# Performance work log

Measured on AMD Instinct MI355X. Metric: run time of the kernel, lower is better.

Reference implementation:

```python
import jax, jax.numpy as jnp
import numpy as np

CHUNK = 32
HEADS = 4
EPS_RMS = 1e-5

def silu(x):
    return jax.nn.silu(x)

def l2norm(x, eps=1e-6):
    return x * jax.lax.rsqrt(jnp.sum(x * x, axis=-1, keepdims=True) + eps)

def short_conv(x, w):
    # x: (b, l, c); w: (c, K) depthwise causal conv, no bias
    K = w.shape[1]
    L = x.shape[1]
    xp = jnp.pad(x, ((0, 0), (K - 1, 0), (0, 0)))
    out = xp[:, 0:L, :] * w[:, 0]
    for k in range(1, K):
        out = out + xp[:, k:k + L, :] * w[:, k]
    return out

def delta_rule_chunkwise(q, k, v, beta, chunk=CHUNK):
    # q,k: (b,h,l,dk); v: (b,h,l,dv); beta: (b,h,l). l divisible by chunk.
    b, h, l, dk = q.shape
    dv = v.shape[-1]
    n = l // chunk
    q = l2norm(q)
    k = l2norm(k)
    v = v * beta[..., None]
    k_beta = k * beta[..., None]
    resh = lambda x: x.reshape(b, h, n, chunk, -1)
    q, k, v, k_beta = map(resh, (q, k, v, k_beta))
    strict_lower = jnp.tril(jnp.ones((chunk, chunk), bool), -1)
    # A = -(k_beta k^T) kept strictly lower triangular
    attn = jnp.where(strict_lower, -(k_beta @ jnp.swapaxes(k, -1, -2)), 0.0)
    # forward substitution: T = (I - A)^{-1} - I built row by row (fixed 32 rows)
    for i in range(1, chunk):
        row = attn[..., i, :]                                  # (b,h,n,c)
        new = attn[..., i, :i] + jnp.einsum('...j,...jk->...k', row, attn[..., :, :i])
        attn = attn.at[..., i, :i].set(new)
    attn = attn + jnp.eye(chunk, dtype=attn.dtype)
    u = attn @ v        # (b,h,n,c,dv)
    w = attn @ k_beta   # (b,h,n,c,dk)
    lower_incl = jnp.tril(jnp.ones((chunk, chunk), bool))
    qc, kc, uc, wc = [jnp.moveaxis(x, 2, 0) for x in (q, k, u, w)]
    S0 = jnp.zeros((b, h, dk, dv), q.dtype)
    def step(S, inp):
        q_i, k_i, u_i, w_i = inp
        attn_i = jnp.where(lower_incl, q_i @ jnp.swapaxes(k_i, -1, -2), 0.0)
        u_adj = u_i - w_i @ S
        o_i = q_i @ S + attn_i @ u_adj
        S = S + jnp.swapaxes(k_i, -1, -2) @ u_adj
        return S, o_i
    S, o = jax.lax.scan(step, S0, (qc, kc, uc, wc))
    o = jnp.moveaxis(o, 0, 2).reshape(b, h, l, dv)
    return o, S

def ema_rule(v, gamma):
    # v: (b,h,l,dv), gamma: (b,h,l); sequential EMA scan
    v_t = jnp.moveaxis(v, 2, 0)       # (l,b,h,dv)
    g_t = jnp.moveaxis(gamma, 2, 0)   # (l,b,h)
    s0 = jnp.zeros(v.shape[:2] + (v.shape[-1],), v.dtype)
    def step(s, inp):
        vt, gt = inp
        s = gt[..., None] * s + (1.0 - gt[..., None]) * vt
        return s, s
    s_fin, out = jax.lax.scan(step, s0, (v_t, g_t))
    return jnp.moveaxis(out, 0, 2), s_fin

def rms_norm(x, w, eps=EPS_RMS):
    return x * jax.lax.rsqrt(jnp.mean(x * x, axis=-1, keepdims=True) + eps) * w

def setup_inputs() -> dict:
    key = jax.random.key(0)
    ks = jax.random.split(key, 16)
    b, l, d = 4, 2048, 1024
    H, conv_K = HEADS, 4
    s = 0.02
    return {
        'hidden_states': jax.random.normal(ks[0], (b, l, d), jnp.float32),
        'Wq': jax.random.normal(ks[1], (d, d), jnp.float32) * s,
        'Wk': jax.random.normal(ks[2], (d, d), jnp.float32) * s,
        'Wv': jax.random.normal(ks[3], (d, d), jnp.float32) * s,
        'conv_q': jax.random.normal(ks[4], (d, conv_K), jnp.float32) * 0.3,
        'conv_k': jax.random.normal(ks[5], (d, conv_K), jnp.float32) * 0.3,
        'conv_v': jax.random.normal(ks[6], (d, conv_K), jnp.float32) * 0.3,
        'Wb': jax.random.normal(ks[7], (d, H), jnp.float32) * s,
        'Wdec': jax.random.normal(ks[8], (d, H), jnp.float32) * s,
        'Wmix': jax.random.normal(ks[9], (d, H), jnp.float32) * s,
        'conv_mix': jax.random.normal(ks[10], (H, conv_K), jnp.float32) * 0.3,
        'mix_bias': jnp.full((H,), -2.0, jnp.float32),
        'rms_w': jnp.ones((d // H,), jnp.float32),
        'Wo': jax.random.normal(ks[11], (d, d), jnp.float32) * s,
    }

def reference(hidden_states, Wq, Wk, Wv, conv_q, conv_k, conv_v, Wb, Wdec, Wmix, conv_mix, mix_bias, rms_w, Wo):
    b, l, d = hidden_states.shape
    H = HEADS
    dk = d // H
    dv = d // H
    # projections + causal depthwise short conv (silu activation inside conv)
    q = silu(short_conv(hidden_states @ Wq, conv_q))
    k = silu(short_conv(hidden_states @ Wk, conv_k))
    v = silu(short_conv(hidden_states @ Wv, conv_v))
    mix_inp = silu(short_conv(hidden_states @ Wmix, conv_mix))  # (b,l,H)
    # qk_activation == 'silu' applies an extra silu after conv (per source)
    q = silu(q)
    k = silu(k)
    # split heads -> (b,H,l,dh)
    to_heads = lambda x, dh: jnp.transpose(x.reshape(b, l, H, dh), (0, 2, 1, 3))
    q_d = to_heads(q, dk)
    k_d = to_heads(k, dk)
    v_d = to_heads(v, dv)
    beta = jax.nn.sigmoid(hidden_states @ Wb)           # (b,l,H)
    beta_d = jnp.transpose(beta, (0, 2, 1))             # (b,H,l)
    o_d, S = delta_rule_chunkwise(q_d, k_d, v_d, beta_d)
    o_d = jnp.transpose(o_d, (0, 2, 1, 3))              # (b,l,H,dv)
    # EMA branch
    gamma = jax.nn.sigmoid(hidden_states @ Wdec)        # (b,l,H)
    gamma_d = jnp.transpose(gamma, (0, 2, 1))
    ema_out, ema_state = ema_rule(v_d, gamma_d)
    ema_out = jnp.transpose(ema_out, (0, 2, 1, 3))      # (b,l,H,dv)
    # fine-grained head mix gate
    mix = jax.nn.sigmoid(mix_inp + mix_bias)            # (b,l,H)
    o = (1.0 - mix[..., None]) * o_d + mix[..., None] * ema_out
    # per-head RMSNorm then output projection
    o = rms_norm(o, rms_w)
    out = o.reshape(b, l, H * dv) @ Wo
    return out
```

## Files before the change

### kernel.cpp

```cpp
#include <hip/hip_runtime.h>
#include <hip/hip_bf16.h>

#define B 4
#define L 2048
#define D 1024
#define NH 4
#define DK 256
#define CHUNK 32
#define NCH 64
#define BH (B*NH)
#define ET 64
#define ENCH (L/ET)
#define TB 8

typedef __attribute__((ext_vector_type(8))) __bf16 bf16x8;
typedef __attribute__((ext_vector_type(4))) __bf16 bf16x4;
typedef __attribute__((ext_vector_type(4))) float f32x4;

__device__ inline unsigned short f2bf(float f) {
    union { float f; unsigned u; } v; v.f = f;
    unsigned r = v.u + 0x7fffu + ((v.u >> 16) & 1u);
    return (unsigned short)(r >> 16);
}
__device__ inline float bf2f(unsigned short h) {
    union { unsigned u; float f; } v; v.u = ((unsigned)h) << 16; return v.f;
}
__device__ inline float sigmoidf_(float x) { return 1.0f / (1.0f + __expf(-x)); }
__device__ inline float siluf_(float x) { return x / (1.0f + __expf(-x)); }

#define MFMA16(a, b, c) __builtin_amdgcn_mfma_f32_16x16x32_bf16((a), (b), (c), 0, 0, 0)

__device__ inline void bar_lds() {
    __builtin_amdgcn_s_waitcnt(0xC07F);
    __builtin_amdgcn_s_barrier();
}

__device__ inline void load_lds16(const unsigned short* g, unsigned short* l) {
    __builtin_amdgcn_global_load_lds(
        (const __attribute__((address_space(1))) unsigned int*)g,
        (__attribute__((address_space(3))) unsigned int*)l, 16, 0, 0);
}

__global__ __launch_bounds__(256) void k_wT(const float* Wq, const float* Wk, const float* Wv,
                                            const float* Wo, unsigned short* wT)
{
    __shared__ float tile[32][33];
    int z = blockIdx.z;
    const float* W = (z == 0) ? Wq : (z == 1) ? Wk : (z == 2) ? Wv : Wo;
    unsigned short* out = wT + (size_t)z * D * D;
    int kt = blockIdx.x * 32, nt = blockIdx.y * 32;
    int tx = threadIdx.x & 31, ty = threadIdx.x >> 5;
#pragma unroll
    for (int i = 0; i < 4; i++)
        tile[ty + 8 * i][tx] = W[(size_t)(kt + ty + 8 * i) * D + nt + tx];
    __syncthreads();
#pragma unroll
    for (int i = 0; i < 4; i++)
        out[(size_t)(nt + ty + 8 * i) * D + kt + tx] = f2bf(tile[tx][ty + 8 * i]);
}

__global__ __launch_bounds__(256) void k_cvt(const float* h, unsigned short* hb, int n4)
{
    int i = blockIdx.x * blockDim.x + threadIdx.x;
    int stride = gridDim.x * blockDim.x;
    const float4* h4 = (const float4*)h;
    for (; i < n4; i += stride) {
        float4 v = h4[i];
        ushort4 o;
        o.x = f2bf(v.x); o.y = f2bf(v.y); o.z = f2bf(v.z); o.w = f2bf(v.w);
        *(ushort4*)(hb + 4 * (size_t)i) = o;
    }
}

template<int NTOT, bool OUT_F32>
__global__ __launch_bounds__(256) void k_gemm_lds(const unsigned short* __restrict__ A,
                                                  const unsigned short* __restrict__ BT,
                                                  void* __restrict__ outp)
{
    __shared__ __align__(16) unsigned short As[128 * 32];
    __shared__ __align__(16) unsigned short Bs[128 * 32];
    const int K = 1024;
    int tid = threadIdx.x;
    int w = tid >> 6, lane = tid & 63;
    int r16 = lane & 15, quad = lane >> 4;
    int wm = w & 1, wn = w >> 1;
    int bm = blockIdx.x * 128;
    int bn = blockIdx.y * 128;
    int lrow = lane >> 2;
    int lcol = (lane & 3) * 8;
    f32x4 z4 = {0.f, 0.f, 0.f, 0.f};
    f32x4 acc[4][4];
#pragma unroll
    for (int i = 0; i < 4; i++)
#pragma unroll
        for (int j = 0; j < 4; j++) acc[i][j] = z4;

    for (int kt = 0; kt < K; kt += 32) {
#pragma unroll
        for (int j = 0; j < 2; j++) {
            int r0 = (w * 2 + j) * 16;
            load_lds16(A + (size_t)(bm + r0 + lrow) * K + kt + lcol, &As[r0 * 32]);
            load_lds16(BT + (size_t)(bn + r0 + lrow) * K + kt + lcol, &Bs[r0 * 32]);
        }
        __syncthreads();
        bf16x8 af[4], bf[4];
#pragma unroll
        for (int ms = 0; ms < 4; ms++)
            af[ms] = *(const bf16x8*)&As[(wm * 64 + ms * 16 + r16) * 32 + quad * 8];
#pragma unroll
        for (int ns = 0; ns < 4; ns++)
            bf[ns] = *(const bf16x8*)&Bs[(wn * 64 + ns * 16 + r16) * 32 + quad * 8];
#pragma unroll
        for (int ms = 0; ms < 4; ms++)
#pragma unroll
            for (int ns = 0; ns < 4; ns++)
                acc[ms][ns] = MFMA16(af[ms], bf[ns], acc[ms][ns]);
        __syncthreads();
    }
#pragma unroll
    for (int ms = 0; ms < 4; ms++)
#pragma unroll
        for (int ns = 0; ns < 4; ns++)
#pragma unroll
            for (int r = 0; r < 4; r++) {
                int m = bm + wm * 64 + ms * 16 + quad * 4 + r;
                int n = bn + wn * 64 + ns * 16 + r16;
                if (OUT_F32)
                    ((float*)outp)[(size_t)m * NTOT + n] = acc[ms][ns][r];
                else
                    ((unsigned short*)outp)[(size_t)m * NTOT + n] = f2bf(acc[ms][ns][r]);
            }
}

__global__ __launch_bounds__(256) void k_smallproj(const float* hid, const float* Wb, const float* Wd,
                                                   const float* Wm, float* beta, float* gamma, float* xmix)
{
    int wave = threadIdx.x >> 6, lane = threadIdx.x & 63;
    int row = blockIdx.x * 4 + wave;
    const float* hrow = hid + (size_t)row * D;
    float acc[12];
#pragma unroll
    for (int j = 0; j < 12; j++) acc[j] = 0.f;
    for (int i = 0; i < 16; i++) {
        int k = lane + 64 * i;
        float h = hrow[k];
        float4 wb = ((const float4*)Wb)[k];
        float4 wd = ((const float4*)Wd)[k];
        float4 wm = ((const float4*)Wm)[k];
        acc[0] += h * wb.x; acc[1] += h * wb.y; acc[2] += h * wb.z; acc[3] += h * wb.w;
        acc[4] += h * wd.x; acc[5] += h * wd.y; acc[6] += h * wd.z; acc[7] += h * wd.w;
        acc[8] += h * wm.x; acc[9] += h * wm.y; acc[10] += h * wm.z; acc[11] += h * wm.w;
    }
#pragma unroll
    for (int j = 0; j < 12; j++)
        for (int off = 32; off; off >>= 1) acc[j] += __shfl_xor(acc[j], off, 64);
    if (lane < 4) {
        beta[(size_t)row * 4 + lane] = sigmoidf_(acc[lane]);
        gamma[(size_t)row * 4 + lane] = sigmoidf_(acc[4 + lane]);
        xmix[(size_t)row * 4 + lane] = acc[8 + lane];
    }
}

__global__ __launch_bounds__(256) void k_convnorm(const unsigned short* __restrict__ xqkv,
                                                  const float* __restrict__ cq,
                                                  const float* __restrict__ ck,
                                                  const float* __restrict__ cv,
                                                  unsigned short* __restrict__ qn,
                                                  unsigned short* __restrict__ kn,
                                                  unsigned short* __restrict__ vb)
{
    int blk = blockIdx.x;
    int b = blk >> 8;
    int t0 = (blk & 255) * TB;
    int tid = threadIdx.x;
    int h = tid >> 6, lane = tid & 63;
    int c = tid * 4;

    float wq[4][4], wk[4][4], wv[4][4];
#pragma unroll
    for (int j = 0; j < 4; j++) {
        float4 a = *(const float4*)(cq + (size_t)(c + j) * 4);
        wq[j][0] = a.x; wq[j][1] = a.y; wq[j][2] = a.z; wq[j][3] = a.w;
        float4 d4 = *(const float4*)(ck + (size_t)(c + j) * 4);
        wk[j][0] = d4.x; wk[j][1] = d4.y; wk[j][2] = d4.z; wk[j][3] = d4.w;
        float4 e = *(const float4*)(cv + (size_t)(c + j) * 4);
        wv[j][0] = e.x; wv[j][1] = e.y; wv[j][2] = e.z; wv[j][3] = e.w;
    }

    float aq[4][4], ak[4][4], av[4][4];
#pragma unroll
    for (int s = 0; s < 4; s++)
#pragma unroll
        for (int j = 0; j < 4; j++) { aq[s][j] = 0.f; ak[s][j] = 0.f; av[s][j] = 0.f; }

    const unsigned short* xb = xqkv + (size_t)(b * L) * (3 * D) + c;

#pragma unroll
    for (int p = 0; p < 3; p++) {
        int r = t0 - 3 + p;
        if (r >= 0) {
            const unsigned short* pp = xb + (size_t)r * (3 * D);
            ushort4 xq = *(const ushort4*)pp;
            ushort4 xk = *(const ushort4*)(pp + D);
            ushort4 xv = *(const ushort4*)(pp + 2 * D);
            float fq[4] = {bf2f(xq.x), bf2f(xq.y), bf2f(xq.z), bf2f(xq.w)};
            float fk[4] = {bf2f(xk.x), bf2f(xk.y), bf2f(xk.z), bf2f(xk.w)};
            float fv[4] = {bf2f(xv.x), bf2f(xv.y), bf2f(xv.z), bf2f(xv.w)};
#pragma unroll
            for (int d = 3 - p; d <= 3; d++) {
                int s = (p + d + 1) & 3;
                int kk = 3 - d;
#pragma unroll
                for (int j = 0; j < 4; j++) {
                    aq[s][j] += wq[j][kk] * fq[j];
                    ak[s][j] += wk[j][kk] * fk[j];
                    av[s][j] += wv[j][kk] * fv[j];
                }
            }
        }
    }

    ushort4 sq2[2], sk2[2], sv2[2];
    {
        const unsigned short* pp = xb + (size_t)t0 * (3 * D);
        sq2[0] = *(const ushort4*)pp;
        sk2[0] = *(const ushort4*)(pp + D);
        sv2[0] = *(const ushort4*)(pp + 2 * D);
    }

#pragma unroll
    for (int i = 0; i < TB; i++) {
        if (i + 1 < TB) {
            const unsigned short* pp = xb + (size_t)(t0 + i + 1) * (3 * D);
            sq2[(i + 1) & 1] = *(const ushort4*)pp;
            sk2[(i + 1) & 1] = *(const ushort4*)(pp + D);
            sv2[(i + 1) & 1] = *(const ushort4*)(pp + 2 * D);
        }
        {
            ushort4 xq = sq2[i & 1], xk = sk2[i & 1], xv = sv2[i & 1];
            float fq[4] = {bf2f(xq.x), bf2f(xq.y), bf2f(xq.z), bf2f(xq.w)};
            float fk[4] = {bf2f(xk.x), bf2f(xk.y), bf2f(xk.z), bf2f(xk.w)};
            float fv[4] = {bf2f(xv.x), bf2f(xv.y), bf2f(xv.z), bf2f(xv.w)};
#pragma unroll
            for (int d = 0; d < 4; d++) {
                if (i + d < TB) {
                    int s = (i + d) & 3;
                    int kk = 3 - d;
#pragma unroll
                    for (int j = 0; j < 4; j++) {
                        aq[s][j] += wq[j][kk] * fq[j];
                        ak[s][j] += wk[j][kk] * fk[j];
                        av[s][j] += wv[j][kk] * fv[j];
                    }
                }
            }
        }
        {
            const int s = i & 3;
            float rq[4], rk[4], rv[4];
#pragma unroll
            for (int j = 0; j < 4; j++) {
                rq[j] = siluf_(siluf_(aq[s][j]));
                rk[j] = siluf_(siluf_(ak[s][j]));
                rv[j] = siluf_(av[s][j]);
            }
            float sqs = rq[0] * rq[0] + rq[1] * rq[1] + rq[2] * rq[2] + rq[3] * rq[3];
            float sks = rk[0] * rk[0] + rk[1] * rk[1] + rk[2] * rk[2] + rk[3] * rk[3];
            for (int off = 32; off; off >>= 1) {
                sqs += __shfl_xor(sqs, off, 64);
                sks += __shfl_xor(sks, off, 64);
            }
            float qs = rsqrtf(sqs + 1e-6f), ks = rsqrtf(sks + 1e-6f);
            int t = t0 + i;
            size_t oidx = ((size_t)(b * NH + h) * L + t) * DK + lane * 4;
            ushort4 oq, ok, ov;
            oq.x = f2bf(rq[0] * qs); oq.y = f2bf(rq[1] * qs); oq.z = f2bf(rq[2] * qs); oq.w = f2bf(rq[3] * qs);
            ok.x = f2bf(rk[0] * ks); ok.y = f2bf(rk[1] * ks); ok.z = f2bf(rk[2] * ks); ok.w = f2bf(rk[3] * ks);
            ov.x = f2bf(rv[0]); ov.y = f2bf(rv[1]); ov.z = f2bf(rv[2]); ov.w = f2bf(rv[3]);
            *(ushort4*)(qn + oidx) = oq;
            *(ushort4*)(kn + oidx) = ok;
            *(ushort4*)(vb + (size_t)(b * L + t) * D + c) = ov;
            if (i + 4 < TB) {
#pragma unroll
                for (int j = 0; j < 4; j++) { aq[s][j] = 0.f; ak[s][j] = 0.f; av[s][j] = 0.f; }
            }
        }
    }
}

__global__ __launch_bounds__(256) void k_convmix(const float* xmix, const float* cmix, float* mixinp)
{
    int idx = blockIdx.x * 256 + threadIdx.x;
    int h = idx & 3;
    int t = (idx >> 2) & (L - 1);
    int b = idx >> 13;
    float acc = 0.f;
#pragma unroll
    for (int kk = 0; kk < 4; kk++) {
        int tt = t - 3 + kk;
        if (tt >= 0) acc += cmix[h * 4 + kk] * xmix[((size_t)(b * L + tt) << 2) + h];
    }
    mixinp[idx] = siluf_(acc);
}

#define KTS 40
__global__ __launch_bounds__(256) void k_delta_pre(const unsigned short* qn, const unsigned short* kn,
                                                   const unsigned short* vb, const float* beta,
                                                   unsigned short* wneg, unsigned short* knT,
                                                   unsigned short* attnb, float* u)
{
    __shared__ __align__(16) unsigned short kTl[256 * KTS];
    __shared__ __align__(16) unsigned short vTl[256 * KTS];
    __shared__ __align__(16) unsigned short T2b[32 * KTS];
    __shared__ float Gs[32 * 33];
    int bx = blockIdx.x;
    int bh = bx >> 6, ch = bx & 63;
    int b = bh >> 2, h = bh & 3;
    int t0 = ch * 32;
    int tid = threadIdx.x;
    int w = tid >> 6, lane = tid & 63;
    int r16 = lane & 15, quad = lane >> 4;
    size_t rowbase = (size_t)(bh * L + t0);
    f32x4 z4 = {0.f, 0.f, 0.f, 0.f};

    if (w < 3) {
        int mi = (w == 0) ? 0 : 1;
        int ni = (w == 2) ? 1 : 0;
        const unsigned short* krm = kn + (rowbase + mi * 16 + r16) * DK;
        const unsigned short* krn = kn + (rowbase + ni * 16 + r16) * DK;
        const unsigned short* qrm = qn + (rowbase + mi * 16 + r16) * DK;
        f32x4 g = z4, qk = z4;
#pragma unroll
        for (int kt = 0; kt < 8; kt++) {
            bf16x8 a  = *(const bf16x8*)(krm + kt * 32 + quad * 8);
            bf16x8 bb = *(const bf16x8*)(krn + kt * 32 + quad * 8);
            bf16x8 qa = *(const bf16x8*)(qrm + kt * 32 + quad * 8);
            g  = MFMA16(a, bb, g);
            qk = MFMA16(qa, bb, qk);
        }
#pragma unroll
        for (int r = 0; r < 4; r++) {
            int i = mi * 16 + quad * 4 + r, j = ni * 16 + r16;
            Gs[i * 33 + j] = g[r];
            attnb[(size_t)(bh * 64 + ch) * 1024 + i * 32 + j] =
                (j <= i) ? f2bf(qk[r]) : (unsigned short)0;
        }
    } else {
#pragma unroll
        for (int r = 0; r < 4; r++) {
            int i = quad * 4 + r, j = 16 + r16;
            attnb[(size_t)(bh * 64 + ch) * 1024 + i * 32 + j] = 0;
        }
    }
    {
        int t = tid & 31, c0 = (tid >> 5) * 32;
        const unsigned short* krow = kn + (rowbase + t) * DK + c0;
        const unsigned short* vrow = vb + ((size_t)(b * L + t0 + t)) * D + h * DK + c0;
#pragma unroll
        for (int j = 0; j < 32; j += 4) {
            ushort4 kv = *(const ushort4*)(krow + j);
            ushort4 vv = *(const ushort4*)(vrow + j);
            kTl[(c0 + j + 0) * KTS + t] = kv.x;
            kTl[(c0 + j + 1) * KTS + t] = kv.y;
            kTl[(c0 + j + 2) * KTS + t] = kv.z;
            kTl[(c0 + j + 3) * KTS + t] = kv.w;
            vTl[(c0 + j + 0) * KTS + t] = vv.x;
            vTl[(c0 + j + 1) * KTS + t] = vv.y;
            vTl[(c0 + j + 2) * KTS + t] = vv.z;
            vTl[(c0 + j + 3) * KTS + t] = vv.w;
        }
    }
    __syncthreads();

    if (w == 0) {
        int c = lane & 31;
        float rr[32];
#pragma unroll
        for (int j = 0; j < 32; j++) rr[j] = Gs[j * 33 + c];
        rr[0] = 0.f;
        float bc = beta[(size_t)(b * L + t0 + c) * NH + h];
#pragma unroll
        for (int i = 1; i < 32; i++) {
            float bi = __shfl(bc, i, 64);
            float s = -bi * rr[i];
#pragma unroll
            for (int j = 1; j < i; j++) {
                float aij = -bi * __shfl(rr[i], j, 64);
                s += aij * ((c < j) ? rr[j] : 0.f);
            }
            rr[i] = (c < i) ? s : 0.f;
        }
        if (lane < 32) {
#pragma unroll
            for (int i = 0; i < 32; i++) {
                float val = (rr[i] + ((i == c) ? 1.f : 0.f)) * bc;
                T2b[i * KTS + c] = f2bf(val);
            }
        }
    } else {
        int idx = tid - 64;
        for (int rowc = idx; rowc < 256; rowc += 192) {
            unsigned short* kT = knT + ((size_t)(bh * 64 + ch) * DK + rowc) * 32;
#pragma unroll
            for (int seg = 0; seg < 4; seg++) {
                uint4 d = *(const uint4*)&kTl[rowc * KTS + seg * 8];
                *(uint4*)(kT + seg * 8) = d;
            }
        }
    }
    __syncthreads();

#pragma unroll
    for (int mt = 0; mt < 2; mt++) {
        bf16x8 ta = *(const bf16x8*)&T2b[(mt * 16 + r16) * KTS + quad * 8];
#pragma unroll
        for (int nt2 = 0; nt2 < 4; nt2++) {
            int nt = w * 4 + nt2;
            bf16x8 vb2 = *(const bf16x8*)&vTl[(nt * 16 + r16) * KTS + quad * 8];
            bf16x8 kb = *(const bf16x8*)&kTl[(nt * 16 + r16) * KTS + quad * 8];
            f32x4 uu = MFMA16(ta, vb2, z4);
            f32x4 ww = MFMA16(ta, kb, z4);
            float* ug = u + (rowbase + mt * 16 + quad * 4) * DK + nt * 16 + r16;
            unsigned short* wg = wneg + (rowbase + mt * 16 + quad * 4) * DK + nt * 16 + r16;
#pragma unroll
            for (int r = 0; r < 4; r++) {
                ug[(size_t)r * DK] = uu[r];
                wg[(size_t)r * DK] = f2bf(-ww[r]);
            }
        }
    }
}

__global__ __launch_bounds__(256) void k_ema_local(const unsigned short* v, const float* gamma,
                                                   float* ema_local, float* Acum,
                                                   float* s_end, float* Pchunk)
{
    __shared__ float gsh[ET];
    int blk = blockIdx.x;
    int bh = blk >> 5;
    int ch = blk & (ENCH - 1);
    int b = bh >> 2, h = bh & 3;
    int c = threadIdx.x;
    int t0 = ch * ET;
    if (c < ET) gsh[c] = gamma[(size_t)(b * L + t0 + c) * NH + h];
    __syncthreads();
    const unsigned short* vg = v + (size_t)(b * L + t0) * D + h * DK + c;
    float* eg = ema_local + (size_t)(b * L + t0) * D + h * DK + c;
    float* Ag = Acum + (size_t)bh * L + t0;
    float s = 0.f;
    float A = 1.f;
#pragma unroll 8
    for (int i = 0; i < ET; i++) {
        float g = gsh[i];
        s = g * s + (1.f - g) * bf2f(vg[(size_t)i * D]);
        A *= g;
        eg[(size_t)i * D] = s;
        if (c == 0) Ag[i] = A;
    }
    s_end[((size_t)bh * ENCH + ch) * DK + c] = s;
    if (c == 0) Pchunk[(size_t)bh * ENCH + ch] = A;
}

__global__ __launch_bounds__(256) void k_ema_carry(const float* s_end, const float* Pchunk, float* S_in)
{
    int bh = blockIdx.x;
    int c = threadIdx.x;
    float S = 0.f;
    for (int ch = 0; ch < ENCH; ch++) {
        S_in[((size_t)bh * ENCH + ch) * DK + c] = S;
        float P = Pchunk[(size_t)bh * ENCH + ch];
        S = P * S + s_end[((size_t)bh * ENCH + ch) * DK + c];
    }
}

#define STS 280
#define USTR 40
__global__ __launch_bounds__(128, 1) void k_scan(const unsigned short* qn, const unsigned short* wneg,
                                                 const unsigned short* knT, const unsigned short* attnb,
                                                 const float* u, float* od)
{
    __shared__ __align__(16) unsigned short st[16 * STS];
    __shared__ __align__(16) unsigned short uat[16 * USTR];
    int bh = blockIdx.x;
    int tile = blockIdx.y;
    int b = bh >> 2, h = bh & 3;
    int mo = threadIdx.x >> 6, lane = threadIdx.x & 63;
    int r16 = lane & 15, quad = lane >> 4;
    int cbase = tile * 16;
    f32x4 z4 = {0.f, 0.f, 0.f, 0.f};
    f32x4 sacc[8];
#pragma unroll
    for (int a = 0; a < 8; a++) sacc[a] = z4;
    const unsigned short* qb = qn + (size_t)bh * L * DK;
    const unsigned short* wb = wneg + (size_t)bh * L * DK;
    const float* ub = u + (size_t)bh * L * DK;
    const unsigned short* kTbase = knT + (size_t)bh * 64 * DK * 32;
    const unsigned short* atbase = attnb + (size_t)bh * 64 * 1024;
    int dkb = mo * 128;

    bf16x8 qf[2][8], wf[2][8];
    f32x4 au0[2];

    auto issue = [&](int ch, int par) {
        int t0 = ch * 32;
        const unsigned short* wrow = wb + (size_t)(t0 + 16 * mo + r16) * DK;
        const unsigned short* qrow = qb + (size_t)(t0 + 16 * mo + r16) * DK;
#pragma unroll
        for (int kt = 0; kt < 8; kt++) {
            qf[par][kt] = *(const bf16x8*)(qrow + kt * 32 + quad * 8);
            wf[par][kt] = *(const bf16x8*)(wrow + kt * 32 + quad * 8);
        }
        const float* up = ub + (size_t)(t0 + 16 * mo + quad * 4) * DK + cbase + r16;
        f32x4 a; a[0] = up[0]; a[1] = up[DK]; a[2] = up[2 * DK]; a[3] = up[3 * DK];
        au0[par] = a;
    };

    issue(0, 0);

    auto body = [&](int ch, int par) {
        int t0 = ch * 32;
        bf16x8 af = *(const bf16x8*)(atbase + (size_t)ch * 1024 + (16 * mo + r16) * 32 + quad * 8);
        const unsigned short* kTb = kTbase + (size_t)ch * DK * 32;
        bf16x8 kf[8];
#pragma unroll
        for (int a = 0; a < 8; a++)
            kf[a] = *(const bf16x8*)(kTb + (size_t)(dkb + a * 16 + r16) * 32 + quad * 8);

#pragma unroll
        for (int a = 0; a < 8; a++) {
            uint2 p;
            p.x = f2bf(sacc[a][0]) | ((unsigned)f2bf(sacc[a][1]) << 16);
            p.y = f2bf(sacc[a][2]) | ((unsigned)f2bf(sacc[a][3]) << 16);
            *(uint2*)&st[r16 * STS + dkb + a * 16 + quad * 4] = p;
        }
        if (ch + 1 < NCH) issue(ch + 1, par ^ 1);
        bar_lds();

        f32x4 au = au0[par], ao = z4;
#pragma unroll
        for (int kt = 0; kt < 8; kt++) {
            bf16x8 sfr = *(const bf16x8*)&st[r16 * STS + kt * 32 + quad * 8];
            au = MFMA16(wf[par][kt], sfr, au);
            ao = MFMA16(qf[par][kt], sfr, ao);
        }
        {
            uint2 p;
            p.x = f2bf(au[0]) | ((unsigned)f2bf(au[1]) << 16);
            p.y = f2bf(au[2]) | ((unsigned)f2bf(au[3]) << 16);
            *(uint2*)&uat[r16 * USTR + 16 * mo + quad * 4] = p;
        }
        bar_lds();

        {
            bf16x8 uf = *(const bf16x8*)&uat[r16 * USTR + quad * 8];
            ao = MFMA16(af, uf, ao);
            float* op = od + (size_t)(b * L + t0 + 16 * mo + quad * 4) * D + h * DK + cbase + r16;
            op[0] = ao[0]; op[D] = ao[1]; op[2 * D] = ao[2]; op[3 * D] = ao[3];
#pragma unroll
            for (int a = 0; a < 8; a++)
                sacc[a] = MFMA16(kf[a], uf, sacc[a]);
        }
    };

    for (int ch2 = 0; ch2 < NCH; ch2 += 2) {
        body(ch2, 0);
        body(ch2 + 1, 1);
    }
}

__global__ __launch_bounds__(256) void k_mixrms(const float* od, const float* ema_local,
                                                const float* Acum, const float* S_in,
                                                const float* mixinp,
                                                const float* mix_bias, const float* rms_w,
                                                unsigned short* onorm)
{
    int row = blockIdx.x;
    int tid = threadIdx.x;
    int h = tid >> 6, lane = tid & 63;
    int b = row >> 11, t = row & (L - 1);
    int bh = b * NH + h;
    int ch = t >> 6;
    float m = sigmoidf_(mixinp[(size_t)row * NH + h] + mix_bias[h]);
    int c = tid * 4;
    float A = Acum[(size_t)bh * L + t];
    float4 sin4 = *(const float4*)(S_in + ((size_t)bh * ENCH + ch) * DK + (c & (DK - 1)));
    float4 o = *(const float4*)(od + (size_t)row * D + c);
    float4 e = *(const float4*)(ema_local + (size_t)row * D + c);
    e.x += A * sin4.x; e.y += A * sin4.y; e.z += A * sin4.z; e.w += A * sin4.w;
    float x0 = o.x + m * (e.x - o.x);
    float x1 = o.y + m * (e.y - o.y);
    float x2 = o.z + m * (e.z - o.z);
    float x3 = o.w + m * (e.w - o.w);
    float ss = x0 * x0 + x1 * x1 + x2 * x2 + x3 * x3;
    for (int off = 32; off; off >>= 1) ss += __shfl_xor(ss, off, 64);
    float scale = rsqrtf(ss * (1.0f / 256.0f) + 1e-5f);
    float4 w = *(const float4*)(rms_w + lane * 4);
    uint2 p;
    p.x = f2bf(x0 * scale * w.x) | ((unsigned)f2bf(x1 * scale * w.y) << 16);
    p.y = f2bf(x2 * scale * w.z) | ((unsigned)f2bf(x3 * scale * w.w) << 16);
    *(uint2*)(onorm + (size_t)row * D + c) = p;
}

extern "C" void kernel_launch(void* const* d_in, const int* in_sizes, int n_in,
                              void* d_out, int out_size, void* d_ws, size_t ws_size,
                              hipStream_t stream)
{
    (void)in_sizes; (void)n_in; (void)out_size; (void)ws_size;
    const float* hidden   = (const float*)d_in[0];
    const float* Wq       = (const float*)d_in[1];
    const float* Wk       = (const float*)d_in[2];
    const float* Wv       = (const float*)d_in[3];
    const float* conv_q   = (const float*)d_in[4];
    const float* conv_k   = (const float*)d_in[5];
    const float* conv_v   = (const float*)d_in[6];
    const float* Wb       = (const float*)d_in[7];
    const float* Wdec     = (const float*)d_in[8];
    const float* Wmix     = (const float*)d_in[9];
    const float* conv_mix = (const float*)d_in[10];
    const float* mix_bias = (const float*)d_in[11];
    const float* rms_w    = (const float*)d_in[12];
    const float* Wo       = (const float*)d_in[13];
    float* out = (float*)d_out;

    char* ws = (char*)d_ws;
    size_t off = 0;
    auto alloc = [&](size_t bytes) -> char* {
        char* p = ws + off;
        off += (bytes + 255) & ~(size_t)255;
        return p;
    };
    unsigned short* wT    = (unsigned short*)alloc((size_t)4 * D * D * 2);
    unsigned short* hidB  = (unsigned short*)alloc((size_t)B * L * D * 2);
    unsigned short* xqkv  = (unsigned short*)alloc((size_t)B * L * 3 * D * 2);
    float* beta   = (float*)alloc((size_t)B * L * NH * 4);
    float* gamma  = (float*)alloc((size_t)B * L * NH * 4);
    float* xmix   = (float*)alloc((size_t)B * L * NH * 4);
    float* mixinp = (float*)alloc((size_t)B * L * NH * 4);
    float* qbuf   = (float*)alloc((size_t)B * L * D * 4);
    float* kbuf   = (float*)alloc((size_t)B * L * D * 4);
    unsigned short* vb = (unsigned short*)alloc((size_t)B * L * D * 2);
    float* u      = (float*)alloc((size_t)B * L * D * 4);
    unsigned short* attnb = (unsigned short*)alloc((size_t)BH * NCH * CHUNK * CHUNK * 2);
    unsigned short* onorm = (unsigned short*)alloc((size_t)B * L * D * 2);
    unsigned short* kn    = (unsigned short*)alloc((size_t)B * L * D * 2);
    unsigned short* qn    = (unsigned short*)alloc((size_t)B * L * D * 2);
    float* Acum   = (float*)alloc((size_t)BH * L * 4);
    float* s_end  = (float*)alloc((size_t)BH * ENCH * DK * 4);
    float* Pchunk = (float*)alloc((size_t)BH * ENCH * 4);
    float* S_in   = (float*)alloc((size_t)BH * ENCH * DK * 4);

    unsigned short* wneg = xqkv + (size_t)B * L * D;
    unsigned short* knT  = xqkv + (size_t)2 * B * L * D;
    float* ema_local = qbuf;
    float* od  = kbuf;

    k_wT<<<dim3(32, 32, 4), 256, 0, stream>>>(Wq, Wk, Wv, Wo, wT);
    k_cvt<<<dim3(2048), 256, 0, stream>>>(hidden, hidB, B * L * D / 4);
    k_gemm_lds<3 * D, false><<<dim3(64, 24), 256, 0, stream>>>(hidB, wT, xqkv);
    k_smallproj<<<dim3(B * L / 4), 256, 0, stream>>>(hidden, Wb, Wdec, Wmix, beta, gamma, xmix);
    k_convnorm<<<dim3(B * L / TB), 256, 0, stream>>>(xqkv, conv_q, conv_k, conv_v, qn, kn, vb);
    k_convmix<<<dim3(B * L * NH / 256), 256, 0, stream>>>(xmix, conv_mix, mixinp);
    k_delta_pre<<<dim3(BH * NCH), 256, 0, stream>>>(qn, kn, vb, beta, wneg, knT, attnb, u);
    k_ema_local<<<dim3(BH * ENCH), 256, 0, stream>>>(vb, gamma, ema_local, Acum, s_end, Pchunk);
    k_ema_carry<<<dim3(BH), 256, 0, stream>>>(s_end, Pchunk, S_in);
    k_scan<<<dim3(16, 16), 128, 0, stream>>>(qn, wneg, knT, attnb, u, od);
    k_mixrms<<<dim3(B * L), 256, 0, stream>>>(od, ema_local, Acum, S_in, mixinp, mix_bias, rms_w, onorm);
    k_gemm_lds<D, true><<<dim3(64, 8), 256, 0, stream>>>(onorm, wT + (size_t)3 * D * D, out);
}
```

Measured before the change: 458.6 us.

## Halve scan column tile width, prefetch k/attn fragments, split MFMA accumulators

The sequential delta-rule scan kernel now uses 8-column value tiles instead of 16, doubling the grid from 256 to 512 blocks so more CUs work on the serial chunk recurrence. Each 16-wide MFMA now carries duplicated columns, and only half the lanes store output. The k-transpose and attention fragments for the next chunk are also prefetched into double-buffered registers. The S·w and S·q reductions are split into even and odd accumulator chains to shorten MFMA dependency chains. In exchange, the redundant per-block loads of q, w and k double total global traffic, and MFMA work is wasted on duplicate columns.

```diff
diff --git a/kernel.cpp b/kernel.cpp
--- a/kernel.cpp
+++ b/kernel.cpp
@@ -12,6 +12,8 @@
 #define ET 64
 #define ENCH (L/ET)
 #define TB 8
+#define TW 8
+#define NTILE (DK/TW)
 
 typedef __attribute__((ext_vector_type(8))) __bf16 bf16x8;
 typedef __attribute__((ext_vector_type(4))) __bf16 bf16x4;
@@ -486,7 +488,7 @@
     int b = bh >> 2, h = bh & 3;
     int mo = threadIdx.x >> 6, lane = threadIdx.x & 63;
     int r16 = lane & 15, quad = lane >> 4;
-    int cbase = tile * 16;
+    int cbase = tile * TW;
     f32x4 z4 = {0.f, 0.f, 0.f, 0.f};
     f32x4 sacc[8];
 #pragma unroll
@@ -498,7 +500,7 @@
     const unsigned short* atbase = attnb + (size_t)bh * 64 * 1024;
     int dkb = mo * 128;
 
-    bf16x8 qf[2][8], wf[2][8];
+    bf16x8 qf[2][8], wf[2][8], kf2[2][8], af2[2];
     f32x4 au0[2];
 
     auto issue = [&](int ch, int par) {
@@ -510,21 +512,25 @@
             qf[par][kt] = *(const bf16x8*)(qrow + kt * 32 + quad * 8);
             wf[par][kt] = *(const bf16x8*)(wrow + kt * 32 + quad * 8);
         }
-        const float* up = ub + (size_t)(t0 + 16 * mo + quad * 4) * DK + cbase + r16;
+        const float* up = ub + (size_t)(t0 + 16 * mo + quad * 4) * DK + cbase + (r16 & (TW - 1));
         f32x4 a; a[0] = up[0]; a[1] = up[DK]; a[2] = up[2 * DK]; a[3] = up[3 * DK];
         au0[par] = a;
     };
 
+    auto loadkf = [&](int ch, int par) {
+        const unsigned short* kTb = kTbase + (size_t)ch * DK * 32;
+#pragma unroll
+        for (int a = 0; a < 8; a++)
+            kf2[par][a] = *(const bf16x8*)(kTb + (size_t)(dkb + a * 16 + r16) * 32 + quad * 8);
+        af2[par] = *(const bf16x8*)(atbase + (size_t)ch * 1024 + (16 * mo + r16) * 32 + quad * 8);
+    };
+
     issue(0, 0);
+    loadkf(0, 0);
 
     auto body = [&](int ch, int par) {
         int t0 = ch * 32;
-        bf16x8 af = *(const bf16x8*)(atbase + (size_t)ch * 1024 + (16 * mo + r16) * 32 + quad * 8);
-        const unsigned short* kTb = kTbase + (size_t)ch * DK * 32;
-        bf16x8 kf[8];
-#pragma unroll
-        for (int a = 0; a < 8; a++)
-            kf[a] = *(const bf16x8*)(kTb + (size_t)(dkb + a * 16 + r16) * 32 + quad * 8);
+        if (ch + 1 < NCH) loadkf(ch + 1, par ^ 1);
 
 #pragma unroll
         for (int a = 0; a < 8; a++) {
@@ -536,13 +542,19 @@
         if (ch + 1 < NCH) issue(ch + 1, par ^ 1);
         bar_lds();
 
-        f32x4 au = au0[par], ao = z4;
-#pragma unroll
-        for (int kt = 0; kt < 8; kt++) {
-            bf16x8 sfr = *(const bf16x8*)&st[r16 * STS + kt * 32 + quad * 8];
-            au = MFMA16(wf[par][kt], sfr, au);
-            ao = MFMA16(qf[par][kt], sfr, ao);
-        }
+        f32x4 au_e = au0[par], au_o = z4, ao_e = z4, ao_o = z4;
+#pragma unroll
+        for (int kt = 0; kt < 8; kt += 2) {
+            bf16x8 s0 = *(const bf16x8*)&st[r16 * STS + (kt + 0) * 32 + quad * 8];
+            bf16x8 s1 = *(const bf16x8*)&st[r16 * STS + (kt + 1) * 32 + quad * 8];
+            au_e = MFMA16(wf[par][kt + 0], s0, au_e);
+            ao_e = MFMA16(qf[par][kt + 0], s0, ao_e);
+            au_o = MFMA16(wf[par][kt + 1], s1, au_o);
+            ao_o = MFMA16(qf[par][kt + 1], s1, ao_o);
+        }
+        f32x4 au = au_e + au_o;
+        f32x4 ao = ao_e + ao_o;
+
         {
             uint2 p;
             p.x = f2bf(au[0]) | ((unsigned)f2bf(au[1]) << 16);
@@ -553,12 +565,14 @@
 
         {
             bf16x8 uf = *(const bf16x8*)&uat[r16 * USTR + quad * 8];
-            ao = MFMA16(af, uf, ao);
-            float* op = od + (size_t)(b * L + t0 + 16 * mo + quad * 4) * D + h * DK + cbase + r16;
-            op[0] = ao[0]; op[D] = ao[1]; op[2 * D] = ao[2]; op[3 * D] = ao[3];
+            ao = MFMA16(af2[par], uf, ao);
+            if (r16 < TW) {
+                float* op = od + (size_t)(b * L + t0 + 16 * mo + quad * 4) * D + h * DK + cbase + r16;
+                op[0] = ao[0]; op[D] = ao[1]; op[2 * D] = ao[2]; op[3 * D] = ao[3];
+            }
 #pragma unroll
             for (int a = 0; a < 8; a++)
-                sacc[a] = MFMA16(kf[a], uf, sacc[a]);
+                sacc[a] = MFMA16(kf2[par][a], uf, sacc[a]);
         }
     };
 
@@ -663,7 +677,7 @@
     k_delta_pre<<<dim3(BH * NCH), 256, 0, stream>>>(qn, kn, vb, beta, wneg, knT, attnb, u);
     k_ema_local<<<dim3(BH * ENCH), 256, 0, stream>>>(vb, gamma, ema_local, Acum, s_end, Pchunk);
     k_ema_carry<<<dim3(BH), 256, 0, stream>>>(s_end, Pchunk, S_in);
-    k_scan<<<dim3(16, 16), 128, 0, stream>>>(qn, wneg, knT, attnb, u, od);
+    k_scan<<<dim3(16, NTILE), 128, 0, stream>>>(qn, wneg, knT, attnb, u, od);
     k_mixrms<<<dim3(B * L), 256, 0, stream>>>(od, ema_local, Acum, S_in, mixinp, mix_bias, rms_w, onorm);
     k_gemm_lds<D, true><<<dim3(64, 8), 256, 0, stream>>>(onorm, wT + (size_t)3 * D * D, out);
 }
```

After: 558.6 us. 21.8% more time.

## Collapse scan kernel to one wavefront per tile, removing block barriers

Applied to the files above, without the earlier changes.

The recurrent delta-rule scan kernel now runs as a single 64-lane wavefront per (head, column tile), holding the full 256-row state slice in registers. Because the LDS exchanges stay inside one wave, the two per-chunk s_barrier syncs and the explicit next-chunk prefetch are dropped. The change also splits the MFMA accumulation chains into even and odd halves for more instruction-level parallelism, and uses the hardware packed bf16 convert instead of software rounding. The cost is half as many threads per block, higher register pressure, and no software prefetch, so global load latency is now exposed on the serial chunk loop.

```diff
diff --git a/kernel.cpp b/kernel.cpp
--- a/kernel.cpp
+++ b/kernel.cpp
@@ -27,13 +27,13 @@
 }
 __device__ inline float sigmoidf_(float x) { return 1.0f / (1.0f + __expf(-x)); }
 __device__ inline float siluf_(float x) { return x / (1.0f + __expf(-x)); }
+__device__ inline unsigned cvt_pk_bf16(float lo, float hi) {
+    unsigned r;
+    asm("v_cvt_pk_bf16_f32 %0, %1, %2" : "=v"(r) : "v"(lo), "v"(hi));
+    return r;
+}
 
 #define MFMA16(a, b, c) __builtin_amdgcn_mfma_f32_16x16x32_bf16((a), (b), (c), 0, 0, 0)
-
-__device__ inline void bar_lds() {
-    __builtin_amdgcn_s_waitcnt(0xC07F);
-    __builtin_amdgcn_s_barrier();
-}
 
 __device__ inline void load_lds16(const unsigned short* g, unsigned short* l) {
     __builtin_amdgcn_global_load_lds(
@@ -475,96 +475,109 @@
 
 #define STS 280
 #define USTR 40
-__global__ __launch_bounds__(128, 1) void k_scan(const unsigned short* qn, const unsigned short* wneg,
-                                                 const unsigned short* knT, const unsigned short* attnb,
-                                                 const float* u, float* od)
+__global__ __launch_bounds__(64, 1) void k_scan(const unsigned short* __restrict__ qn,
+                                                const unsigned short* __restrict__ wneg,
+                                                const unsigned short* __restrict__ knT,
+                                                const unsigned short* __restrict__ attnb,
+                                                const float* __restrict__ u, float* __restrict__ od)
 {
     __shared__ __align__(16) unsigned short st[16 * STS];
     __shared__ __align__(16) unsigned short uat[16 * USTR];
     int bh = blockIdx.x;
     int tile = blockIdx.y;
     int b = bh >> 2, h = bh & 3;
-    int mo = threadIdx.x >> 6, lane = threadIdx.x & 63;
-    int r16 = lane & 15, quad = lane >> 4;
+    int lane = threadIdx.x;
+    int n = lane & 15, q = lane >> 4;
     int cbase = tile * 16;
     f32x4 z4 = {0.f, 0.f, 0.f, 0.f};
-    f32x4 sacc[8];
-#pragma unroll
-    for (int a = 0; a < 8; a++) sacc[a] = z4;
+    f32x4 Sacc[16];
+#pragma unroll
+    for (int i = 0; i < 16; i++) Sacc[i] = z4;
+
     const unsigned short* qb = qn + (size_t)bh * L * DK;
     const unsigned short* wb = wneg + (size_t)bh * L * DK;
     const float* ub = u + (size_t)bh * L * DK;
     const unsigned short* kTbase = knT + (size_t)bh * 64 * DK * 32;
     const unsigned short* atbase = attnb + (size_t)bh * 64 * 1024;
-    int dkb = mo * 128;
-
-    bf16x8 qf[2][8], wf[2][8];
-    f32x4 au0[2];
-
-    auto issue = [&](int ch, int par) {
+
+#pragma unroll 1
+    for (int ch = 0; ch < NCH; ++ch) {
         int t0 = ch * 32;
-        const unsigned short* wrow = wb + (size_t)(t0 + 16 * mo + r16) * DK;
-        const unsigned short* qrow = qb + (size_t)(t0 + 16 * mo + r16) * DK;
-#pragma unroll
-        for (int kt = 0; kt < 8; kt++) {
-            qf[par][kt] = *(const bf16x8*)(qrow + kt * 32 + quad * 8);
-            wf[par][kt] = *(const bf16x8*)(wrow + kt * 32 + quad * 8);
-        }
-        const float* up = ub + (size_t)(t0 + 16 * mo + quad * 4) * DK + cbase + r16;
-        f32x4 a; a[0] = up[0]; a[1] = up[DK]; a[2] = up[2 * DK]; a[3] = up[3 * DK];
-        au0[par] = a;
-    };
-
-    issue(0, 0);
-
-    auto body = [&](int ch, int par) {
-        int t0 = ch * 32;
-        bf16x8 af = *(const bf16x8*)(atbase + (size_t)ch * 1024 + (16 * mo + r16) * 32 + quad * 8);
-        const unsigned short* kTb = kTbase + (size_t)ch * DK * 32;
-        bf16x8 kf[8];
-#pragma unroll
-        for (int a = 0; a < 8; a++)
-            kf[a] = *(const bf16x8*)(kTb + (size_t)(dkb + a * 16 + r16) * 32 + quad * 8);
-
-#pragma unroll
-        for (int a = 0; a < 8; a++) {
+        bf16x8 wf[2][8], qf[2][8];
+#pragma unroll
+        for (int mt = 0; mt < 2; mt++) {
+            const unsigned short* wr = wb + (size_t)(t0 + 16 * mt + n) * DK + q * 8;
+            const unsigned short* qr = qb + (size_t)(t0 + 16 * mt + n) * DK + q * 8;
+#pragma unroll
+            for (int kt = 0; kt < 8; kt++) {
+                wf[mt][kt] = *(const bf16x8*)(wr + kt * 32);
+                qf[mt][kt] = *(const bf16x8*)(qr + kt * 32);
+            }
+        }
+        bf16x8 kf[16];
+        {
+            const unsigned short* kTb = kTbase + (size_t)ch * DK * 32 + n * 32 + q * 8;
+#pragma unroll
+            for (int i = 0; i < 16; i++)
+                kf[i] = *(const bf16x8*)(kTb + i * 16 * 32);
+        }
+        bf16x8 af[2];
+#pragma unroll
+        for (int mt = 0; mt < 2; mt++)
+            af[mt] = *(const bf16x8*)(atbase + (size_t)ch * 1024 + (16 * mt + n) * 32 + q * 8);
+        f32x4 uB[2];
+#pragma unroll
+        for (int mt = 0; mt < 2; mt++) {
+            const float* up = ub + (size_t)(t0 + 16 * mt + q * 4) * DK + cbase + n;
+#pragma unroll
+            for (int r = 0; r < 4; r++) uB[mt][r] = up[(size_t)r * DK];
+        }
+
+#pragma unroll
+        for (int i = 0; i < 16; i++) {
             uint2 p;
-            p.x = f2bf(sacc[a][0]) | ((unsigned)f2bf(sacc[a][1]) << 16);
-            p.y = f2bf(sacc[a][2]) | ((unsigned)f2bf(sacc[a][3]) << 16);
-            *(uint2*)&st[r16 * STS + dkb + a * 16 + quad * 4] = p;
-        }
-        if (ch + 1 < NCH) issue(ch + 1, par ^ 1);
-        bar_lds();
-
-        f32x4 au = au0[par], ao = z4;
-#pragma unroll
-        for (int kt = 0; kt < 8; kt++) {
-            bf16x8 sfr = *(const bf16x8*)&st[r16 * STS + kt * 32 + quad * 8];
-            au = MFMA16(wf[par][kt], sfr, au);
-            ao = MFMA16(qf[par][kt], sfr, ao);
-        }
-        {
+            p.x = cvt_pk_bf16(Sacc[i][0], Sacc[i][1]);
+            p.y = cvt_pk_bf16(Sacc[i][2], Sacc[i][3]);
+            *(uint2*)&st[n * STS + i * 16 + q * 4] = p;
+        }
+
+        f32x4 auE[2], auO[2], aoE[2], aoO[2];
+#pragma unroll
+        for (int mt = 0; mt < 2; mt++) { auE[mt] = uB[mt]; auO[mt] = z4; aoE[mt] = z4; aoO[mt] = z4; }
+#pragma unroll
+        for (int kt = 0; kt < 8; kt += 2) {
+            bf16x8 s0 = *(const bf16x8*)&st[n * STS + (kt + 0) * 32 + q * 8];
+            bf16x8 s1 = *(const bf16x8*)&st[n * STS + (kt + 1) * 32 + q * 8];
+#pragma unroll
+            for (int mt = 0; mt < 2; mt++) {
+                auE[mt] = MFMA16(wf[mt][kt + 0], s0, auE[mt]);
+                aoE[mt] = MFMA16(qf[mt][kt + 0], s0, aoE[mt]);
+                auO[mt] = MFMA16(wf[mt][kt + 1], s1, auO[mt]);
+                aoO[mt] = MFMA16(qf[mt][kt + 1], s1, aoO[mt]);
+            }
+        }
+
+#pragma unroll
+        for (int mt = 0; mt < 2; mt++) {
+            f32x4 au = auE[mt] + auO[mt];
             uint2 p;
-            p.x = f2bf(au[0]) | ((unsigned)f2bf(au[1]) << 16);
-            p.y = f2bf(au[2]) | ((unsigned)f2bf(au[3]) << 16);
-            *(uint2*)&uat[r16 * USTR + 16 * mo + quad * 4] = p;
-        }
-        bar_lds();
-
-        {
-            bf16x8 uf = *(const bf16x8*)&uat[r16 * USTR + quad * 8];
-            ao = MFMA16(af, uf, ao);
-            float* op = od + (size_t)(b * L + t0 + 16 * mo + quad * 4) * D + h * DK + cbase + r16;
+            p.x = cvt_pk_bf16(au[0], au[1]);
+            p.y = cvt_pk_bf16(au[2], au[3]);
+            *(uint2*)&uat[n * USTR + 16 * mt + q * 4] = p;
+        }
+        bf16x8 uf = *(const bf16x8*)&uat[n * USTR + q * 8];
+
+#pragma unroll
+        for (int mt = 0; mt < 2; mt++) {
+            f32x4 ao = aoE[mt] + aoO[mt];
+            ao = MFMA16(af[mt], uf, ao);
+            float* op = od + (size_t)(b * L + t0 + 16 * mt + q * 4) * D + h * DK + cbase + n;
             op[0] = ao[0]; op[D] = ao[1]; op[2 * D] = ao[2]; op[3 * D] = ao[3];
-#pragma unroll
-            for (int a = 0; a < 8; a++)
-                sacc[a] = MFMA16(kf[a], uf, sacc[a]);
-        }
-    };
-
-    for (int ch2 = 0; ch2 < NCH; ch2 += 2) {
-        body(ch2, 0);
-        body(ch2 + 1, 1);
+        }
+
+#pragma unroll
+        for (int i = 0; i < 16; i++)
+            Sacc[i] = MFMA16(kf[i], uf, Sacc[i]);
     }
 }
 
@@ -663,7 +676,7 @@
     k_delta_pre<<<dim3(BH * NCH), 256, 0, stream>>>(qn, kn, vb, beta, wneg, knT, attnb, u);
     k_ema_local<<<dim3(BH * ENCH), 256, 0, stream>>>(vb, gamma, ema_local, Acum, s_end, Pchunk);
     k_ema_carry<<<dim3(BH), 256, 0, stream>>>(s_end, Pchunk, S_in);
-    k_scan<<<dim3(16, 16), 128, 0, stream>>>(qn, wneg, knT, attnb, u, od);
+    k_scan<<<dim3(16, 16), 64, 0, stream>>>(qn, wneg, knT, attnb, u, od);
     k_mixrms<<<dim3(B * L), 256, 0, stream>>>(od, ema_local, Acum, S_in, mixinp, mix_bias, rms_w, onorm);
     k_gemm_lds<D, true><<<dim3(64, 8), 256, 0, stream>>>(onorm, wT + (size_t)3 * D * D, out);
 }
```

Measured after the change: 536.4 us. +17.0%, slower.

## Stage q/w chunks into swizzled LDS via async loads and prefetch k/attn fragments

Applied to the files above, without the earlier changes.

The scan kernel now double-buffers the q and w chunk tiles in LDS using direct global-to-LDS loads with an XOR swizzle, instead of holding them in registers. It also prefetches the next chunk's k^T and attention fragments into registers, splits the S-product accumulation into even and odd chains to shorten MFMA dependency chains, and uses a packed bf16 convert instruction. The aim is to hide global memory latency behind the serial chunk recurrence and reduce register pressure. In exchange it adds 64KB of LDS and a full vmcnt(0) wait at the top of each chunk, and the bf16 rounding may differ slightly.

```diff
diff --git a/kernel.cpp b/kernel.cpp
--- a/kernel.cpp
+++ b/kernel.cpp
@@ -27,6 +27,11 @@
 }
 __device__ inline float sigmoidf_(float x) { return 1.0f / (1.0f + __expf(-x)); }
 __device__ inline float siluf_(float x) { return x / (1.0f + __expf(-x)); }
+__device__ inline unsigned cvt_pk_bf16(float lo, float hi) {
+    unsigned r;
+    asm("v_cvt_pk_bf16_f32 %0, %1, %2" : "=v"(r) : "v"(lo), "v"(hi));
+    return r;
+}
 
 #define MFMA16(a, b, c) __builtin_amdgcn_mfma_f32_16x16x32_bf16((a), (b), (c), 0, 0, 0)
 
@@ -475,22 +480,27 @@
 
 #define STS 280
 #define USTR 40
-__global__ __launch_bounds__(128, 1) void k_scan(const unsigned short* qn, const unsigned short* wneg,
-                                                 const unsigned short* knT, const unsigned short* attnb,
-                                                 const float* u, float* od)
+__global__ __launch_bounds__(128, 1) void k_scan(const unsigned short* __restrict__ qn,
+                                                 const unsigned short* __restrict__ wneg,
+                                                 const unsigned short* __restrict__ knT,
+                                                 const unsigned short* __restrict__ attnb,
+                                                 const float* __restrict__ u, float* __restrict__ od)
 {
     __shared__ __align__(16) unsigned short st[16 * STS];
     __shared__ __align__(16) unsigned short uat[16 * USTR];
+    __shared__ __align__(16) unsigned short sq[2][32 * 256];
+    __shared__ __align__(16) unsigned short sw[2][32 * 256];
     int bh = blockIdx.x;
     int tile = blockIdx.y;
     int b = bh >> 2, h = bh & 3;
     int mo = threadIdx.x >> 6, lane = threadIdx.x & 63;
-    int r16 = lane & 15, quad = lane >> 4;
+    int n = lane & 15, q = lane >> 4;
     int cbase = tile * 16;
     f32x4 z4 = {0.f, 0.f, 0.f, 0.f};
     f32x4 sacc[8];
 #pragma unroll
     for (int a = 0; a < 8; a++) sacc[a] = z4;
+
     const unsigned short* qb = qn + (size_t)bh * L * DK;
     const unsigned short* wb = wneg + (size_t)bh * L * DK;
     const float* ub = u + (size_t)bh * L * DK;
@@ -498,67 +508,89 @@
     const unsigned short* atbase = attnb + (size_t)bh * 64 * 1024;
     int dkb = mo * 128;
 
-    bf16x8 qf[2][8], wf[2][8];
-    f32x4 au0[2];
-
-    auto issue = [&](int ch, int par) {
-        int t0 = ch * 32;
-        const unsigned short* wrow = wb + (size_t)(t0 + 16 * mo + r16) * DK;
-        const unsigned short* qrow = qb + (size_t)(t0 + 16 * mo + r16) * DK;
-#pragma unroll
-        for (int kt = 0; kt < 8; kt++) {
-            qf[par][kt] = *(const bf16x8*)(qrow + kt * 32 + quad * 8);
-            wf[par][kt] = *(const bf16x8*)(wrow + kt * 32 + quad * 8);
-        }
-        const float* up = ub + (size_t)(t0 + 16 * mo + quad * 4) * DK + cbase + r16;
+    int hl = lane >> 5, cc = lane & 31;
+    auto stage = [&](int ch, int p) {
+        const unsigned short* src = (mo == 0) ? (qb + (size_t)ch * 32 * DK)
+                                              : (wb + (size_t)ch * 32 * DK);
+        unsigned short* dst = (mo == 0) ? sq[p] : sw[p];
+#pragma unroll
+        for (int seg = 0; seg < 16; seg++) {
+            int row = seg * 2 + hl;
+            int scol = cc ^ (row & 7);
+            load_lds16(src + (size_t)row * DK + scol * 8, dst + seg * 512);
+        }
+    };
+
+    f32x4 uB[2];
+    auto loadu = [&](int ch, int p) {
+        const float* up = ub + (size_t)(ch * 32 + 16 * mo + q * 4) * DK + cbase + n;
         f32x4 a; a[0] = up[0]; a[1] = up[DK]; a[2] = up[2 * DK]; a[3] = up[3 * DK];
-        au0[par] = a;
+        uB[p] = a;
     };
 
-    issue(0, 0);
+    bf16x8 kf2[2][8], af2[2];
+    auto loadkf = [&](int ch, int p) {
+        const unsigned short* kTb = kTbase + (size_t)ch * DK * 32;
+#pragma unroll
+        for (int a = 0; a < 8; a++)
+            kf2[p][a] = *(const bf16x8*)(kTb + (size_t)(dkb + a * 16 + n) * 32 + q * 8);
+        af2[p] = *(const bf16x8*)(atbase + (size_t)ch * 1024 + (16 * mo + n) * 32 + q * 8);
+    };
+
+    stage(0, 0); loadu(0, 0); loadkf(0, 0);
 
     auto body = [&](int ch, int par) {
         int t0 = ch * 32;
-        bf16x8 af = *(const bf16x8*)(atbase + (size_t)ch * 1024 + (16 * mo + r16) * 32 + quad * 8);
-        const unsigned short* kTb = kTbase + (size_t)ch * DK * 32;
-        bf16x8 kf[8];
-#pragma unroll
-        for (int a = 0; a < 8; a++)
-            kf[a] = *(const bf16x8*)(kTb + (size_t)(dkb + a * 16 + r16) * 32 + quad * 8);
-
+        asm volatile("s_waitcnt vmcnt(0)" ::: "memory");
+        if (ch + 1 < NCH) {
+            stage(ch + 1, par ^ 1);
+            loadu(ch + 1, par ^ 1);
+            loadkf(ch + 1, par ^ 1);
+        }
 #pragma unroll
         for (int a = 0; a < 8; a++) {
-            uint2 p;
-            p.x = f2bf(sacc[a][0]) | ((unsigned)f2bf(sacc[a][1]) << 16);
-            p.y = f2bf(sacc[a][2]) | ((unsigned)f2bf(sacc[a][3]) << 16);
-            *(uint2*)&st[r16 * STS + dkb + a * 16 + quad * 4] = p;
-        }
-        if (ch + 1 < NCH) issue(ch + 1, par ^ 1);
+            uint2 pk2;
+            pk2.x = cvt_pk_bf16(sacc[a][0], sacc[a][1]);
+            pk2.y = cvt_pk_bf16(sacc[a][2], sacc[a][3]);
+            *(uint2*)&st[n * STS + dkb + a * 16 + q * 4] = pk2;
+        }
         bar_lds();
 
-        f32x4 au = au0[par], ao = z4;
-#pragma unroll
-        for (int kt = 0; kt < 8; kt++) {
-            bf16x8 sfr = *(const bf16x8*)&st[r16 * STS + kt * 32 + quad * 8];
-            au = MFMA16(wf[par][kt], sfr, au);
-            ao = MFMA16(qf[par][kt], sfr, ao);
-        }
+        f32x4 auE = uB[par], auO = z4, aoE = z4, aoO = z4;
+        int rowoff = (16 * mo + n) * 256;
+        int rsw = n & 7;
+#pragma unroll
+        for (int kt = 0; kt < 8; kt += 2) {
+            bf16x8 s0 = *(const bf16x8*)&st[n * STS + (kt + 0) * 32 + q * 8];
+            bf16x8 s1 = *(const bf16x8*)&st[n * STS + (kt + 1) * 32 + q * 8];
+            bf16x8 w0 = *(const bf16x8*)&sw[par][rowoff + (((kt + 0) * 4 + q) ^ rsw) * 8];
+            bf16x8 q0 = *(const bf16x8*)&sq[par][rowoff + (((kt + 0) * 4 + q) ^ rsw) * 8];
+            bf16x8 w1 = *(const bf16x8*)&sw[par][rowoff + (((kt + 1) * 4 + q) ^ rsw) * 8];
+            bf16x8 q1 = *(const bf16x8*)&sq[par][rowoff + (((kt + 1) * 4 + q) ^ rsw) * 8];
+            auE = MFMA16(w0, s0, auE);
+            aoE = MFMA16(q0, s0, aoE);
+            auO = MFMA16(w1, s1, auO);
+            aoO = MFMA16(q1, s1, aoO);
+        }
+        f32x4 au = auE + auO;
+
         {
-            uint2 p;
-            p.x = f2bf(au[0]) | ((unsigned)f2bf(au[1]) << 16);
-            p.y = f2bf(au[2]) | ((unsigned)f2bf(au[3]) << 16);
-            *(uint2*)&uat[r16 * USTR + 16 * mo + quad * 4] = p;
+            uint2 pu;
+            pu.x = cvt_pk_bf16(au[0], au[1]);
+            pu.y = cvt_pk_bf16(au[2], au[3]);
+            *(uint2*)&uat[n * USTR + 16 * mo + q * 4] = pu;
         }
         bar_lds();
 
         {
-            bf16x8 uf = *(const bf16x8*)&uat[r16 * USTR + quad * 8];
-            ao = MFMA16(af, uf, ao);
-            float* op = od + (size_t)(b * L + t0 + 16 * mo + quad * 4) * D + h * DK + cbase + r16;
+            bf16x8 uf = *(const bf16x8*)&uat[n * USTR + q * 8];
+            f32x4 ao = aoE + aoO;
+            ao = MFMA16(af2[par], uf, ao);
+            float* op = od + (size_t)(b * L + t0 + 16 * mo + q * 4) * D + h * DK + cbase + n;
             op[0] = ao[0]; op[D] = ao[1]; op[2 * D] = ao[2]; op[3 * D] = ao[3];
 #pragma unroll
             for (int a = 0; a < 8; a++)
-                sacc[a] = MFMA16(kf[a], uf, sacc[a]);
+                sacc[a] = MFMA16(kf2[par][a], uf, sacc[a]);
         }
     };
 
```

Measured after the change: 475.0 us. +3.6%, slower.
